# Performance work log

Measured on AMD Instinct MI355X. Metric: run time of the kernel, lower is better.

Reference implementation:

```python
import jax, jax.numpy as jnp
import numpy as np

FEATURE_SIZE = 128
STRIDE = 16
BASE_SIZE = 16
RATIOS = [0.5, 1, 2]
SCALES = [8, 16, 32]


def _generate_anchors(feature_size, stride):
    # Faithful to the torch module's numpy anchor generation (incl. rounding).
    size = BASE_SIZE * BASE_SIZE
    size_ratios = size / np.array(RATIOS)
    ws = np.round(np.sqrt(size_ratios))
    hs = np.round(ws * np.array(RATIOS))
    base = []
    for w, h in zip(ws, hs):
        for s in SCALES:
            base.append([0.0, 0.0, w * s, h * s])
    base = np.array(base)  # [9, 4]
    xo, yo = np.meshgrid(np.arange(feature_size), np.arange(feature_size), indexing='ij')
    # original loop order: x outer, y inner, then 9 base anchors
    centers = np.stack([xo * stride, yo * stride], axis=-1).reshape(-1, 1, 2)  # [F*F,1,2]
    wh = np.broadcast_to(base[None, :, 2:4], (feature_size * feature_size, 9, 2))
    anchors = np.concatenate([np.broadcast_to(centers, wh.shape), wh], axis=-1).reshape(-1, 4)
    return jnp.asarray(anchors, dtype=jnp.float32)  # [F*F*9, 4]


def _conv(x, w, b, pad):
    y = jax.lax.conv_general_dilated(
        x, w, window_strides=(1, 1), padding=[(pad, pad), (pad, pad)],
        dimension_numbers=('NCHW', 'OIHW', 'NCHW'))
    return y + b[None, :, None, None]


def setup_inputs() -> dict:
    key = jax.random.key(0)
    ks = jax.random.split(key, 4)
    F = FEATURE_SIZE
    x = jax.random.normal(ks[0], (1, 1024, F, F), dtype=jnp.float32)
    base_w = jax.random.normal(ks[1], (512, 1024, 3, 3), dtype=jnp.float32) * 0.01
    base_b = jnp.zeros((512,), dtype=jnp.float32)
    cls_w = jax.random.normal(ks[2], (18, 512, 1, 1), dtype=jnp.float32) * 0.01
    cls_b = jnp.zeros((18,), dtype=jnp.float32)
    reg_w = jax.random.normal(ks[3], (36, 512, 1, 1), dtype=jnp.float32) * 0.01
    reg_b = jnp.zeros((36,), dtype=jnp.float32)
    return {"x": x, "base_w": base_w, "base_b": base_b,
            "cls_w": cls_w, "cls_b": cls_b, "reg_w": reg_w, "reg_b": reg_b}


def reference(x, base_w, base_b, cls_w, cls_b, reg_w, reg_b):
    F = FEATURE_SIZE
    anchors = _generate_anchors(F, STRIDE)  # [N,4], N = F*F*9

    rpn_conv = jax.nn.relu(_conv(x, base_w, base_b, pad=1))        # [1,512,F,F]
    rpn_cls = _conv(rpn_conv, cls_w, cls_b, pad=0)                  # [1,18,F,F]
    # softmax over the 2-way fg/bg axis after reshape, as in the original
    cls_rs = rpn_cls.reshape(1, 2, 9 * F, F)
    cls_prob = jax.nn.softmax(cls_rs, axis=1).reshape(1, 18, F, F)
    rpn_reg = _conv(rpn_conv, reg_w, reg_b, pad=0)                  # [1,36,F,F]

    cls = jnp.transpose(cls_prob, (0, 2, 3, 1)).reshape(-1, 2)      # [N,2]
    reg = jnp.transpose(rpn_reg, (0, 2, 3, 1)).reshape(-1, 4)       # [N,4]

    # Vectorized decode — faithful to the original per-anchor loop math:
    # p0 = ax + aw*d0 ; p1 = ay + ah*d1 ; p2 = aw + exp(d2) ; p3 = ah + exp(d3)
    p0 = anchors[:, 0] + anchors[:, 2] * reg[:, 0]
    p1 = anchors[:, 1] + anchors[:, 3] * reg[:, 1]
    p2 = anchors[:, 2] + jnp.exp(reg[:, 2])
    p3 = anchors[:, 3] + jnp.exp(reg[:, 3])
    proposals = jnp.stack([p0, p1, p2, p3], axis=-1)                # [N,4]
    scores = cls[:, 1]                                              # [N]
    return jnp.concatenate([proposals, scores[:, None]], axis=-1)   # [N,5]
```

## Files before the change

kernel.cpp:

```cpp
#include <hip/hip_runtime.h>
#include <hip/hip_bf16.h>

typedef unsigned short u16;
typedef short s4v __attribute__((ext_vector_type(4)));
typedef short s8v __attribute__((ext_vector_type(8)));
typedef float f4v __attribute__((ext_vector_type(4)));

#define F 128
#define CIN 1024
#define CMID 512
#define XP 130
#define K9 9216

#define A_ELEMS 8704
#define B_ELEMS 8192
#define AOFF(b) ((b) * A_ELEMS)
#define BOFF(b) (2 * A_ELEMS + (b) * B_ELEMS)

__device__ __forceinline__ u16 f2bf(float v) {
    union { float f; unsigned u; } x; x.f = v;
    unsigned r = x.u + 0x7fff + ((x.u >> 16) & 1);
    return (u16)(r >> 16);
}

__device__ __forceinline__ void gl16(const u16* g, u16* l) {
    __builtin_amdgcn_global_load_lds(
        (const __attribute__((address_space(1))) void*)g,
        (__attribute__((address_space(3))) void*)l,
        16, 0, 0);
}

__constant__ float WBASE[9] = {184.f, 368.f, 736.f, 128.f, 256.f, 512.f,  88.f, 176.f, 352.f};
__constant__ float HBASE[9] = { 96.f, 192.f, 384.f, 128.f, 256.f, 512.f, 176.f, 352.f, 704.f};

__global__ __launch_bounds__(256) void prep_all(
    const float* __restrict__ x, const float* __restrict__ bw,
    const float* __restrict__ cls_w, const float* __restrict__ reg_w,
    u16* __restrict__ xpad, u16* __restrict__ wt, u16* __restrict__ wc) {
    __shared__ u16 ldsT[64 * 132];
    const int b = blockIdx.x;
    const int tid = threadIdx.x;

    if (b < 2048) {
        const int h  = b >> 4;
        const int cb = (b & 15) * 64;
        {
            const int L = tid & 31, cl = tid >> 5;
            const int w4 = L * 4;
            #pragma unroll
            for (int p = 0; p < 8; ++p) {
                const int c = p * 8 + cl;
                f4v v = *(const f4v*)&x[(cb + c) * (F * F) + h * F + w4];
                s4v pk;
                #pragma unroll
                for (int k = 0; k < 4; ++k) pk[k] = (short)f2bf(v[k]);
                *(s4v*)&ldsT[c * 132 + w4] = pk;
            }
        }
        __syncthreads();
        {
            const int cs = (tid & 7) * 8;
            const int wb = tid >> 3;
            #pragma unroll
            for (int p = 0; p < 4; ++p) {
                const int w = p * 32 + wb;
                s8v o;
                #pragma unroll
                for (int j = 0; j < 8; ++j) o[j] = (short)ldsT[(cs + j) * 132 + w];
                *(s8v*)&xpad[((h + 1) * XP + (w + 1)) * CIN + cb + cs] = o;
            }
        }
    } else if (b < 2560) {
        const int oc = b - 2048;
        #pragma unroll 1
        for (int p = 0; p < 4; ++p) {
            const int c = p * 256 + tid;
            const float* src = bw + oc * K9 + c * 9;
            #pragma unroll
            for (int q = 0; q < 9; ++q)
                wt[oc * K9 + q * 1024 + c] = f2bf(src[q]);
        }
    } else if (b < 2818) {
        int t = (b - 2560) * 256 + tid;
        int cell = t >> 7, c8 = (t & 127) * 8;
        int h, w;
        if (cell < 130)      { h = 0;   w = cell; }
        else if (cell < 260) { h = 129; w = cell - 130; }
        else { int rm = cell - 260; h = 1 + (rm >> 1); w = (rm & 1) * 129; }
        s8v z = {};
        *(s8v*)&xpad[(h * XP + w) * CIN + c8] = z;
    } else {
        int t = (b - 2818) * 256 + tid;
        int oc = t >> 9, c = t & 511;
        float v = 0.f;
        if (oc < 18)      v = cls_w[oc * 512 + c];
        else if (oc < 54) v = reg_w[(oc - 18) * 512 + c];
        wc[t] = f2bf(v);
    }
}

__global__ __launch_bounds__(256, 2) void gemm_conv(
    const u16* __restrict__ xpad, const u16* __restrict__ wt,
    const float* __restrict__ bias, u16* __restrict__ rpn) {
    __shared__ u16 smem[2 * A_ELEMS + 2 * B_ELEMS];
    const int tid = threadIdx.x;
    const int w_id = (blockIdx.x & 7) * 64 + (blockIdx.x >> 3);
    const int oc0 = ((w_id & 7) >> 1) * 128;
    const int gh  = (w_id >> 3) * 2 + (w_id & 1);

    const int lane = tid & 63;
    const int wv = tid >> 6;
    const int lm = lane & 15;
    const int lq = lane >> 4;
    const int wm = (wv >> 1) * 64;
    const int wn = (wv & 1) * 64;

    const int sw = (lane & 7) ^ ((lane >> 3) & 7);
    const u16* pA = xpad + (lane >> 3) * CIN + sw * 8;
    const u16* pB = wt + (size_t)(oc0 + wv * 32 + (lane >> 3)) * K9 + sw * 8;

    f4v acc[4][4] = {};

    auto issueA = [&](int ms) {
        const int dy = ms >> 4, cc = ms & 15;
        const u16* src = pA + ((gh + dy) * XP) * CIN + cc * 64;
        u16* dst = &smem[AOFF(ms & 1)];
        #pragma unroll
        for (int jj = 0; jj < 4; ++jj) {
            const int ci = wv * 4 + jj;
            gl16(src + ci * 8 * CIN, dst + ci * 512);
        }
        if (wv == 0) gl16(src + 16 * 8 * CIN, dst + 16 * 512);
    };
    auto issueB = [&](int ms, int dx, int buf) {
        const int dy = ms >> 4, cc = ms & 15;
        const int dydx = dy * 3 + dx;
        const u16* src = pB + dydx * CIN + cc * 64;
        u16* dst = &smem[BOFF(buf) + wv * 32 * 64];
        #pragma unroll
        for (int jj = 0; jj < 4; ++jj)
            gl16(src + jj * 8 * K9, dst + jj * 8 * 64);
    };

    issueA(0);
    issueB(0, 0, 0);
    __syncthreads();

    int t = 0;
    for (int ms = 0; ms < 48; ++ms) {
        const u16* Ab = &smem[AOFF(ms & 1)];
        #pragma unroll
        for (int dx = 0; dx < 3; ++dx, ++t) {
            if (t + 1 < 144) {
                const int msn = (dx == 2) ? ms + 1 : ms;
                const int dxn = (dx == 2) ? 0 : dx + 1;
                issueB(msn, dxn, (t + 1) & 1);
            }
            if (dx == 0 && ms + 1 < 48) issueA(ms + 1);
            const u16* Bb = &smem[BOFF(t & 1)];
            #pragma unroll
            for (int kk = 0; kk < 2; ++kk) {
                const int kseg = kk * 4 + lq;
                s8v af[4], bfr[4];
                #pragma unroll
                for (int i = 0; i < 4; ++i) {
                    const int ra = wm + i * 16 + lm + dx;
                    const int rb = wn + i * 16 + lm;
                    af[i]  = *(const s8v*)&Ab[ra * 64 + ((kseg ^ (ra & 7)) << 3)];
                    bfr[i] = *(const s8v*)&Bb[rb * 64 + ((kseg ^ (rb & 7)) << 3)];
                }
                #pragma unroll
                for (int mi = 0; mi < 4; ++mi)
                    #pragma unroll
                    for (int ni = 0; ni < 4; ++ni)
                        acc[mi][ni] = __builtin_amdgcn_mfma_f32_16x16x32_bf16(
                            af[mi], bfr[ni], acc[mi][ni], 0, 0, 0);
            }
            __syncthreads();
        }
    }

    #pragma unroll
    for (int ni = 0; ni < 4; ++ni) {
        const int oc = oc0 + wn + ni * 16 + lm;
        const float bv = bias[oc];
        #pragma unroll
        for (int mi = 0; mi < 4; ++mi) {
            #pragma unroll
            for (int rr = 0; rr < 4; ++rr) {
                const int m = wm + mi * 16 + lq * 4 + rr;
                float v = acc[mi][ni][rr] + bv;
                v = v > 0.f ? v : 0.f;
                rpn[(gh * 128 + m) * CMID + oc] = f2bf(v);
            }
        }
    }
}

__global__ __launch_bounds__(256) void stage23(
    const u16* __restrict__ rpn, const u16* __restrict__ wc,
    const float* __restrict__ cls_b, const float* __restrict__ reg_b,
    float* __restrict__ out) {
    __shared__ float part[4][32][65];
    const int tid = threadIdx.x, lane = tid & 63, wv = tid >> 6;
    const int lm = lane & 15, lq = lane >> 4;
    const int m0 = blockIdx.x * 32;

    #pragma unroll
    for (int g = 0; g < 2; ++g) {
        f4v acc[4] = {};
        const u16* arow = rpn + (m0 + g * 16 + lm) * CMID + wv * 128 + lq * 8;
        const u16* brow = wc + lm * CMID + wv * 128 + lq * 8;
        #pragma unroll
        for (int k = 0; k < 4; ++k) {
            s8v af = *(const s8v*)(arow + k * 32);
            #pragma unroll
            for (int ni = 0; ni < 4; ++ni) {
                s8v bf = *(const s8v*)(brow + ni * 16 * CMID + k * 32);
                acc[ni] = __builtin_amdgcn_mfma_f32_16x16x32_bf16(af, bf, acc[ni], 0, 0, 0);
            }
        }
        #pragma unroll
        for (int ni = 0; ni < 4; ++ni)
            #pragma unroll
            for (int rr = 0; rr < 4; ++rr)
                part[wv][g * 16 + lq * 4 + rr][ni * 16 + lm] = acc[ni][rr];
    }
    __syncthreads();

    float vsum[8];
    const int col = tid & 63, rb = tid >> 6;
    const float bv = col < 18 ? cls_b[col] : (col < 54 ? reg_b[col - 18] : 0.f);
    #pragma unroll
    for (int rr = 0; rr < 8; ++rr) {
        const int row = rb * 8 + rr;
        vsum[rr] = part[0][row][col] + part[1][row][col]
                 + part[2][row][col] + part[3][row][col] + bv;
    }
    __syncthreads();
    #pragma unroll
    for (int rr = 0; rr < 8; ++rr)
        part[0][rb * 8 + rr][col] = vsum[rr];
    __syncthreads();

    #pragma unroll 1
    for (int g = 0; g < 2; ++g) {
        if (tid < 144) {
            const int pl0 = tid / 9, a = tid - pl0 * 9;
            const int pl = g * 16 + pl0;
            const float* v = part[0][pl];
            const int ch = 2 * a + 1;
            const int pair = (ch < 9) ? ch + 9 : ch - 9;
            const float score = 1.f / (1.f + expf(v[pair] - v[ch]));
            const float r0 = v[18 + 4 * a], r1 = v[19 + 4 * a];
            const float r2 = v[20 + 4 * a], r3 = v[21 + 4 * a];
            const float wb = WBASE[a], hb = HBASE[a];
            const int p = m0 + pl;
            const int h = p >> 7, w = p & 127;
            float* o = out + (p * 9 + a) * 5;
            o[0] = h * 16.f + wb * r0;
            o[1] = w * 16.f + hb * r1;
            o[2] = wb + expf(r2);
            o[3] = hb + expf(r3);
            o[4] = score;
        }
    }
}

extern "C" void kernel_launch(void* const* d_in, const int* in_sizes, int n_in,
                              void* d_out, int out_size, void* d_ws, size_t ws_size,
                              hipStream_t stream) {
    const float* x      = (const float*)d_in[0];
    const float* base_w = (const float*)d_in[1];
    const float* base_b = (const float*)d_in[2];
    const float* cls_w  = (const float*)d_in[3];
    const float* cls_b  = (const float*)d_in[4];
    const float* reg_w  = (const float*)d_in[5];
    const float* reg_b  = (const float*)d_in[6];
    float* out = (float*)d_out;

    char* ws = (char*)d_ws;
    u16* xpad = (u16*)ws;
    u16* wt   = (u16*)(ws + 34611200);
    u16* wc   = (u16*)(ws + 34611200 + 9437184);
    u16* rpn  = (u16*)(ws + 34611200 + 9437184 + 65536);

    prep_all<<<2946, 256, 0, stream>>>(x, base_w, cls_w, reg_w, xpad, wt, wc);
    gemm_conv<<<512, 256, 0, stream>>>(xpad, wt, base_b, rpn);
    stage23<<<512, 256, 0, stream>>>(rpn, wc, cls_b, reg_b, out);
}
```

Before: 259.7 us.

## Enlarge conv GEMM tile to 128x256 with triple-buffered B and manual vmcnt waits

The 3x3 conv GEMM goes from 256-thread blocks computing 128x128 tiles to 512-thread blocks computing 128x256 tiles, halving the grid. Each A (input row) tile is now shared across twice as many output channels. B weight tiles move to a three-stage ring with prefetch distance two. The per-step __syncthreads is replaced by explicit s_waitcnt vmcnt counts plus s_barrier, and s_setprio is raised around the MFMA block. This aims to raise data reuse and overlap loads with compute, at the cost of larger LDS use, one block per CU, and hand-tuned wait counts that must match the exact number of issued loads.

```diff
diff --git a/kernel.cpp b/kernel.cpp
--- a/kernel.cpp
+++ b/kernel.cpp
@@ -13,7 +13,7 @@
 #define K9 9216
 
 #define A_ELEMS 8704
-#define B_ELEMS 8192
+#define B_ELEMS 16384
 #define AOFF(b) ((b) * A_ELEMS)
 #define BOFF(b) (2 * A_ELEMS + (b) * B_ELEMS)
 
@@ -99,21 +99,21 @@
     }
 }
 
-__global__ __launch_bounds__(256, 2) void gemm_conv(
+__global__ __launch_bounds__(512, 1) void gemm_conv(
     const u16* __restrict__ xpad, const u16* __restrict__ wt,
     const float* __restrict__ bias, u16* __restrict__ rpn) {
-    __shared__ u16 smem[2 * A_ELEMS + 2 * B_ELEMS];
+    __shared__ u16 smem[2 * A_ELEMS + 3 * B_ELEMS];
     const int tid = threadIdx.x;
-    const int w_id = (blockIdx.x & 7) * 64 + (blockIdx.x >> 3);
-    const int oc0 = ((w_id & 7) >> 1) * 128;
-    const int gh  = (w_id >> 3) * 2 + (w_id & 1);
+    const int w_id = (blockIdx.x & 7) * 32 + (blockIdx.x >> 3);
+    const int oc0 = (w_id & 1) * 256;
+    const int gh  = w_id >> 1;
 
     const int lane = tid & 63;
     const int wv = tid >> 6;
     const int lm = lane & 15;
     const int lq = lane >> 4;
-    const int wm = (wv >> 1) * 64;
-    const int wn = (wv & 1) * 64;
+    const int wm = (wv >> 2) * 64;
+    const int wn = (wv & 3) * 64;
 
     const int sw = (lane & 7) ^ ((lane >> 3) & 7);
     const u16* pA = xpad + (lane >> 3) * CIN + sw * 8;
@@ -126,38 +126,50 @@
         const u16* src = pA + ((gh + dy) * XP) * CIN + cc * 64;
         u16* dst = &smem[AOFF(ms & 1)];
         #pragma unroll
-        for (int jj = 0; jj < 4; ++jj) {
-            const int ci = wv * 4 + jj;
+        for (int jj = 0; jj < 2; ++jj) {
+            const int ci = wv * 2 + jj;
             gl16(src + ci * 8 * CIN, dst + ci * 512);
         }
         if (wv == 0) gl16(src + 16 * 8 * CIN, dst + 16 * 512);
     };
-    auto issueB = [&](int ms, int dx, int buf) {
+    auto issueB = [&](int t2) {
+        const int ms = t2 / 3, dx = t2 % 3;
         const int dy = ms >> 4, cc = ms & 15;
         const int dydx = dy * 3 + dx;
         const u16* src = pB + dydx * CIN + cc * 64;
-        u16* dst = &smem[BOFF(buf) + wv * 32 * 64];
+        u16* dst = &smem[BOFF(t2 % 3) + wv * 32 * 64];
         #pragma unroll
         for (int jj = 0; jj < 4; ++jj)
             gl16(src + jj * 8 * K9, dst + jj * 8 * 64);
     };
 
     issueA(0);
-    issueB(0, 0, 0);
-    __syncthreads();
-
-    int t = 0;
+    issueB(0);
+    issueB(1);
+
     for (int ms = 0; ms < 48; ++ms) {
         const u16* Ab = &smem[AOFF(ms & 1)];
         #pragma unroll
-        for (int dx = 0; dx < 3; ++dx, ++t) {
-            if (t + 1 < 144) {
-                const int msn = (dx == 2) ? ms + 1 : ms;
-                const int dxn = (dx == 2) ? 0 : dx + 1;
-                issueB(msn, dxn, (t + 1) & 1);
-            }
+        for (int dx = 0; dx < 3; ++dx) {
+            const int t = ms * 3 + dx;
+
+            if (dx == 0) {
+                asm volatile("s_waitcnt vmcnt(4)" ::: "memory");
+            } else if (ms < 47) {
+                if (wv == 0) asm volatile("s_waitcnt vmcnt(7)" ::: "memory");
+                else         asm volatile("s_waitcnt vmcnt(6)" ::: "memory");
+            } else if (dx == 1) {
+                asm volatile("s_waitcnt vmcnt(4)" ::: "memory");
+            } else {
+                asm volatile("s_waitcnt vmcnt(0)" ::: "memory");
+            }
+            __builtin_amdgcn_s_barrier();
+
+            if (t + 2 < 144) issueB(t + 2);
             if (dx == 0 && ms + 1 < 48) issueA(ms + 1);
-            const u16* Bb = &smem[BOFF(t & 1)];
+
+            const u16* Bb = &smem[BOFF(dx)];
+            __builtin_amdgcn_s_setprio(1);
             #pragma unroll
             for (int kk = 0; kk < 2; ++kk) {
                 const int kseg = kk * 4 + lq;
@@ -176,7 +188,7 @@
                         acc[mi][ni] = __builtin_amdgcn_mfma_f32_16x16x32_bf16(
                             af[mi], bfr[ni], acc[mi][ni], 0, 0, 0);
             }
-            __syncthreads();
+            __builtin_amdgcn_s_setprio(0);
         }
     }
 
@@ -286,6 +298,6 @@
     u16* rpn  = (u16*)(ws + 34611200 + 9437184 + 65536);
 
     prep_all<<<2946, 256, 0, stream>>>(x, base_w, cls_w, reg_w, xpad, wt, wc);
-    gemm_conv<<<512, 256, 0, stream>>>(xpad, wt, base_b, rpn);
+    gemm_conv<<<256, 512, 0, stream>>>(xpad, wt, base_b, rpn);
     stage23<<<512, 256, 0, stream>>>(rpn, wc, cls_b, reg_b, out);
 }
```

Measured after the change: 259.1 us. Within noise of the previous version (-0.3%).
